# Performance work log

Measured on AMD Instinct MI355X. Metric: run time of the kernel, lower is better.

## Reference

```python
import jax, jax.numpy as jnp
import numpy as np

IN_FEATURES = 1024
OUT_FEATURES = 1024


def setup_inputs() -> dict:
    key = jax.random.key(0)
    k_x, k_w, k_b = jax.random.split(key, 3)
    # input activations [batch, seq, in_features]
    x = jax.random.normal(k_x, (4, 8192, IN_FEATURES), dtype=jnp.float32)
    # kaiming_uniform_(a=sqrt(5)) on [out, in] -> bound = 1/sqrt(in_features)
    bound = 1.0 / np.sqrt(IN_FEATURES)
    weight = jax.random.uniform(k_w, (OUT_FEATURES, IN_FEATURES), dtype=jnp.float32,
                                minval=-bound, maxval=bound)
    bias = jax.random.uniform(k_b, (OUT_FEATURES,), dtype=jnp.float32,
                              minval=-bound, maxval=bound)
    # adiabatic binarization scale factors (non-trainable scalars)
    kk = jnp.float32(10.0)
    aa = jnp.float32(1.0)
    return {"x": x, "weight": weight, "bias": bias, "kk": kk, "aa": aa}


def reference(x, weight, bias, kk, aa):
    # BinaryLinearFunction: soft-binarize the weight with learned scales, then GEMM.
    # w_bin = aa * clamp(kk * w, -1, 1)  (annealed binarization; kk -> inf gives sign(w))
    w_bin = aa * jnp.clip(kk * weight, -1.0, 1.0)  # [out, in]
    # out[b, s, o] = sum_i x[b, s, i] * w_bin[o, i] + bias[o]
    return jnp.einsum('bsi,oi->bso', x, w_bin) + bias
```

## Files before the change

### kernel.cpp

```cpp
#include <hip/hip_runtime.h>
#include <stdint.h>

#define K_DIM 1024
#define N_DIM 1024
#define BM 256
#define BN 256
#define BK 64
#define NK (K_DIM / BK)

typedef __attribute__((ext_vector_type(4))) float f32x4;
typedef __attribute__((ext_vector_type(8))) short bf16x8;
typedef __attribute__((ext_vector_type(4))) uint32_t u32x4;

__device__ __forceinline__ uint32_t pack_bf16(float a, float b) {
  uint32_t ua = __builtin_bit_cast(uint32_t, a) + 0x8000u;
  uint32_t ub = __builtin_bit_cast(uint32_t, b) + 0x8000u;
  return __builtin_amdgcn_perm(ub, ua, 0x07060302u);
}

__device__ __forceinline__ float wbin1(float v, float kkv, float aav) {
  float t = v * kkv;
  t = fminf(fmaxf(t, -1.0f), 1.0f);
  return t * aav;
}

__global__ __launch_bounds__(256) void wconv(const float* __restrict__ w,
                                             const float* __restrict__ kkp,
                                             const float* __restrict__ aap,
                                             uint32_t* __restrict__ wb) {
  const float kkv = kkp[0];
  const float aav = aap[0];
  const int g = blockIdx.x * 256 + threadIdx.x;
  const f32x4* src = (const f32x4*)(w + (size_t)g * 16);
  f32x4 v0 = src[0], v1 = src[1], v2 = src[2], v3 = src[3];
  uint32_t p[8];
#pragma unroll
  for (int i = 0; i < 4; ++i) {
    f32x4 v = i == 0 ? v0 : (i == 1 ? v1 : (i == 2 ? v2 : v3));
    p[2 * i] = pack_bf16(wbin1(v[0], kkv, aav), wbin1(v[1], kkv, aav));
    p[2 * i + 1] = pack_bf16(wbin1(v[2], kkv, aav), wbin1(v[3], kkv, aav));
  }
  u32x4* dst = (u32x4*)(wb + (size_t)g * 8);
  dst[0] = u32x4{p[0], p[1], p[2], p[3]};
  dst[1] = u32x4{p[4], p[5], p[6], p[7]};
}

__global__ __launch_bounds__(256) void xconv(const float* __restrict__ x,
                                             uint32_t* __restrict__ xb) {
  const size_t g = (size_t)blockIdx.x * 256 + threadIdx.x;
  const f32x4* src = (const f32x4*)(x + g * 16);
  f32x4 v0 = src[0], v1 = src[1], v2 = src[2], v3 = src[3];
  uint32_t p[8];
  p[0] = pack_bf16(v0[0], v0[1]); p[1] = pack_bf16(v0[2], v0[3]);
  p[2] = pack_bf16(v1[0], v1[1]); p[3] = pack_bf16(v1[2], v1[3]);
  p[4] = pack_bf16(v2[0], v2[1]); p[5] = pack_bf16(v2[2], v2[3]);
  p[6] = pack_bf16(v3[0], v3[1]); p[7] = pack_bf16(v3[2], v3[3]);
  u32x4* dst = (u32x4*)(xb + g * 8);
  dst[0] = u32x4{p[0], p[1], p[2], p[3]};
  dst[1] = u32x4{p[4], p[5], p[6], p[7]};
}

__global__ __launch_bounds__(512, 2) void binlin_gemm8(
    const uint32_t* __restrict__ xb, const uint32_t* __restrict__ wb,
    const float* __restrict__ bias, float* __restrict__ out) {
  __shared__ uint32_t lds[2][(BM + BN) * 32];

  const int tid = threadIdx.x;

  const int per = gridDim.x >> 3;
  const int logical = (blockIdx.x & 7) * per + (blockIdx.x >> 3);
  const int mIdx = logical >> 2;
  const int nIdx = logical & 3;
  const int row0 = mIdx * BM;
  const int col0 = nIdx * BN;

  const int w8 = tid >> 6;
  const int lane = tid & 63;
  const int brow = lane >> 3;
  const int bslot = (lane & 7) ^ brow;
  const uint32_t* ga_base =
      xb + (size_t)(row0 + w8 * 32 + brow) * (K_DIM / 2) + bslot * 4;
  const uint32_t* gb_base =
      wb + (size_t)(col0 + w8 * 32 + brow) * (K_DIM / 2) + bslot * 4;

  const int wr = w8 >> 2;
  const int wc = w8 & 3;
  const int cl = lane & 15;
  const int kg = lane >> 4;

  f32x4 acc[8][4] = {};
  bf16x8 af[2][4], bfr[2][2];

#define STAGE_A8(kt, dstbase)                                             \
  do {                                                                    \
    _Pragma("unroll") for (int c4 = 0; c4 < 4; ++c4) {                    \
      __builtin_amdgcn_global_load_lds(                                   \
          (const __attribute__((address_space(1))) uint32_t*)(            \
              ga_base + (size_t)(c4 * 8) * (K_DIM / 2) + (kt) * 32),      \
          (__attribute__((address_space(3))) uint32_t*)(                  \
              (dstbase) + (w8 * 32 + c4 * 8) * 32),                       \
          16, 0, 0);                                                      \
    }                                                                     \
  } while (0)

#define STAGE_B8(kt, dstbase)                                             \
  do {                                                                    \
    _Pragma("unroll") for (int c4 = 0; c4 < 4; ++c4) {                    \
      __builtin_amdgcn_global_load_lds(                                   \
          (const __attribute__((address_space(1))) uint32_t*)(            \
              gb_base + (size_t)(c4 * 8) * (K_DIM / 2) + (kt) * 32),      \
          (__attribute__((address_space(3))) uint32_t*)(                  \
              (dstbase) + BM * 32 + (w8 * 32 + c4 * 8) * 32),             \
          16, 0, 0);                                                      \
    }                                                                     \
  } while (0)

#define READ_AF(AB, MH)                                                        \
  _Pragma("unroll") for (int ks = 0; ks < 2; ++ks)                             \
  _Pragma("unroll") for (int m = 0; m < 4; ++m) {                              \
    int rr = wr * 128 + ((MH)*4 + m) * 16 + cl;                                \
    af[ks][m] =                                                                \
        *(const bf16x8*)((AB) + rr * 32 + (((ks * 4 + kg) ^ (rr & 7)) * 4));   \
  }

#define READ_BF(BB, NH)                                                        \
  _Pragma("unroll") for (int ks = 0; ks < 2; ++ks)                             \
  _Pragma("unroll") for (int n = 0; n < 2; ++n) {                              \
    int rr = wc * 64 + ((NH)*2 + n) * 16 + cl;                                 \
    bfr[ks][n] =                                                               \
        *(const bf16x8*)((BB) + rr * 32 + (((ks * 4 + kg) ^ (rr & 7)) * 4));   \
  }

#define PHTAIL(MH, NH)                                                         \
  __builtin_amdgcn_s_barrier();                                                \
  asm volatile("s_waitcnt lgkmcnt(0)" ::: "memory");                           \
  __builtin_amdgcn_sched_barrier(0);                                           \
  __builtin_amdgcn_s_setprio(1);                                               \
  _Pragma("unroll") for (int ks = 0; ks < 2; ++ks)                             \
  _Pragma("unroll") for (int m = 0; m < 4; ++m)                                \
  _Pragma("unroll") for (int n = 0; n < 2; ++n)                                \
  acc[(MH)*4 + m][(NH)*2 + n] = __builtin_amdgcn_mfma_f32_16x16x32_bf16(       \
      af[ks][m], bfr[ks][n], acc[(MH)*4 + m][(NH)*2 + n], 0, 0, 0);            \
  __builtin_amdgcn_s_setprio(0);

  STAGE_A8(0, &lds[0][0]);
  STAGE_B8(0, &lds[0][0]);
  asm volatile("s_waitcnt vmcnt(0)" ::: "memory");
  __builtin_amdgcn_s_barrier();

  for (int kt = 0; kt < NK; ++kt) {
    const uint32_t* AB = &lds[kt & 1][0];
    const uint32_t* BB = AB + BM * 32;
    uint32_t* ND = &lds[(kt & 1) ^ 1][0];
    const bool more = (kt + 1) < NK;
    READ_AF(AB, 0);
    READ_BF(BB, 0);
    if (more) STAGE_A8(kt + 1, ND);
    PHTAIL(0, 0);
    __builtin_amdgcn_s_barrier();
    READ_BF(BB, 1);
    if (more) STAGE_B8(kt + 1, ND);
    PHTAIL(0, 1);
    __builtin_amdgcn_s_barrier();
    READ_AF(AB, 1);
    PHTAIL(1, 1);
    __builtin_amdgcn_s_barrier();
    READ_BF(BB, 0);
    PHTAIL(1, 0);
    asm volatile("s_waitcnt vmcnt(0)" ::: "memory");
    __builtin_amdgcn_s_barrier();
  }

#pragma unroll
  for (int n = 0; n < 4; ++n) {
    int col = col0 + wc * 64 + n * 16 + cl;
    float bv = bias[col];
#pragma unroll
    for (int m = 0; m < 8; ++m) {
      int rowb = row0 + wr * 128 + m * 16 + kg * 4;
#pragma unroll
      for (int i = 0; i < 4; ++i) {
        out[(size_t)(rowb + i) * N_DIM + col] = acc[m][n][i] + bv;
      }
    }
  }
#undef STAGE_A8
#undef STAGE_B8
#undef READ_AF
#undef READ_BF
#undef PHTAIL
}

__global__ __launch_bounds__(512, 2) void binlin_gemm_fb(
    const float* __restrict__ x, const uint32_t* __restrict__ wb,
    const float* __restrict__ bias, float* __restrict__ out) {
  __shared__ uint32_t lds[2][(BM + BN) * 32];

  const int tid = threadIdx.x;
  const int per = gridDim.x >> 3;
  const int logical = (blockIdx.x & 7) * per + (blockIdx.x >> 3);
  const int mIdx = logical >> 2;
  const int nIdx = logical & 3;
  const int row0 = mIdx * BM;
  const int col0 = nIdx * BN;

  const int r = tid >> 1;
  const int h = tid & 1;
  const int sw = r & 7;
  const float* ga = x + (size_t)(row0 + r) * K_DIM + h * 32;
  const int aoff = r * 32;

  const int w8 = tid >> 6;
  const int lane = tid & 63;
  const int brow = lane >> 3;
  const int bslot = (lane & 7) ^ brow;
  const uint32_t* gb_base =
      wb + (size_t)(col0 + w8 * 32 + brow) * (K_DIM / 2) + bslot * 4;
  const int boff = (w8 * 32) * 32;

  const int wr = w8 >> 2;
  const int wc = w8 & 3;
  const int cl = lane & 15;
  const int kg = lane >> 4;

  f32x4 acc[8][4] = {};
  f32x4 ra[8];

#define LOADA(kt)                                                \
  {                                                              \
    const f32x4* pa = (const f32x4*)(ga + (kt)*BK);              \
    _Pragma("unroll") for (int i = 0; i < 8; ++i) ra[i] = pa[i]; \
  }
#define WRITEA(buf)                                                       \
  {                                                                       \
    uint32_t* lap = &lds[buf][0] + aoff;                                  \
    _Pragma("unroll") for (int j = 0; j < 4; ++j) {                       \
      u32x4 pk = {pack_bf16(ra[2 * j][0], ra[2 * j][1]),                  \
                  pack_bf16(ra[2 * j][2], ra[2 * j][3]),                  \
                  pack_bf16(ra[2 * j + 1][0], ra[2 * j + 1][1]),          \
                  pack_bf16(ra[2 * j + 1][2], ra[2 * j + 1][3])};         \
      *(u32x4*)(lap + (((h * 4 + j) ^ sw) * 4)) = pk;                     \
    }                                                                     \
  }
#define STAGEB(kt, buf)                                                    \
  {                                                                        \
    uint32_t* lbp = &lds[buf][BM * 32] + boff;                             \
    _Pragma("unroll") for (int c = 0; c < 4; ++c) {                        \
      __builtin_amdgcn_global_load_lds(                                    \
          (const __attribute__((address_space(1))) uint32_t*)(             \
              gb_base + (size_t)(c * 8) * (K_DIM / 2) + (kt)*32),          \
          (__attribute__((address_space(3))) uint32_t*)(lbp + c * 8 * 32), \
          16, 0, 0);                                                       \
    }                                                                      \
  }
#define COMPUTE(buf)                                                           \
  {                                                                            \
    const uint32_t* A = &lds[buf][0];                                          \
    const uint32_t* B = &lds[buf][BM * 32];                                    \
    _Pragma("unroll") for (int ks = 0; ks < 2; ++ks) {                         \
      bf16x8 bfr[4];                                                           \
      _Pragma("unroll") for (int n = 0; n < 4; ++n) {                          \
        int rr = wc * 64 + n * 16 + cl;                                        \
        bfr[n] =                                                               \
            *(const bf16x8*)(B + rr * 32 + (((ks * 4 + kg) ^ (rr & 7)) * 4));  \
      }                                                                        \
      _Pragma("unroll") for (int mh = 0; mh < 2; ++mh) {                       \
        bf16x8 af[4];                                                          \
        _Pragma("unroll") for (int m = 0; m < 4; ++m) {                        \
          int rr = wr * 128 + (mh * 4 + m) * 16 + cl;                          \
          af[m] =                                                              \
              *(const bf16x8*)(A + rr * 32 + (((ks * 4 + kg) ^ (rr & 7)) * 4));\
        }                                                                      \
        __builtin_amdgcn_s_setprio(1);                                         \
        _Pragma("unroll") for (int m = 0; m < 4; ++m)                          \
            _Pragma("unroll") for (int n = 0; n < 4; ++n)                      \
                acc[mh * 4 + m][n] = __builtin_amdgcn_mfma_f32_16x16x32_bf16(  \
                    af[m], bfr[n], acc[mh * 4 + m][n], 0, 0, 0);               \
        __builtin_amdgcn_s_setprio(0);                                         \
      }                                                                        \
    }                                                                          \
  }

  LOADA(0);
  STAGEB(0, 0);
  WRITEA(0);
  asm volatile("s_waitcnt vmcnt(0) lgkmcnt(0)" ::: "memory");
  __builtin_amdgcn_s_barrier();

  for (int kt2 = 0; kt2 < NK; kt2 += 2) {
    LOADA(kt2 + 1);
    STAGEB(kt2 + 1, 1);
    asm volatile("s_waitcnt vmcnt(12)" ::: "memory");
    __builtin_amdgcn_s_barrier();
    __builtin_amdgcn_sched_barrier(0);
    COMPUTE(0);
    WRITEA(1);
    asm volatile("s_waitcnt lgkmcnt(0)" ::: "memory");
    if (kt2 + 2 < NK) {
      LOADA(kt2 + 2);
      STAGEB(kt2 + 2, 0);
      asm volatile("s_waitcnt vmcnt(12)" ::: "memory");
    } else {
      asm volatile("s_waitcnt vmcnt(0)" ::: "memory");
    }
    __builtin_amdgcn_s_barrier();
    __builtin_amdgcn_sched_barrier(0);
    COMPUTE(1);
    if (kt2 + 2 < NK) {
      WRITEA(0);
      asm volatile("s_waitcnt lgkmcnt(0)" ::: "memory");
    }
  }

#pragma unroll
  for (int n = 0; n < 4; ++n) {
    int col = col0 + wc * 64 + n * 16 + cl;
    float bv = bias[col];
#pragma unroll
    for (int m = 0; m < 8; ++m) {
      int rowb = row0 + wr * 128 + m * 16 + kg * 4;
#pragma unroll
      for (int i = 0; i < 4; ++i) {
        out[(size_t)(rowb + i) * N_DIM + col] = acc[m][n][i] + bv;
      }
    }
  }
#undef LOADA
#undef WRITEA
#undef STAGEB
#undef COMPUTE
}

extern "C" void kernel_launch(void* const* d_in, const int* in_sizes, int n_in,
                              void* d_out, int out_size, void* d_ws, size_t ws_size,
                              hipStream_t stream) {
  const float* x = (const float*)d_in[0];
  const float* w = (const float*)d_in[1];
  const float* bias = (const float*)d_in[2];
  const float* kk = (const float*)d_in[3];
  const float* aa = (const float*)d_in[4];
  float* out = (float*)d_out;

  uint32_t* wb = (uint32_t*)d_ws;
  wconv<<<(N_DIM * K_DIM) / (256 * 16), 256, 0, stream>>>(w, kk, aa, wb);

  const int M = in_sizes[0] / K_DIM;
  const int grid = (M / BM) * (N_DIM / BN);

  const size_t wb_bytes = (size_t)N_DIM * K_DIM * 2;
  const size_t xb_bytes = (size_t)M * K_DIM * 2;
  if (ws_size >= wb_bytes + xb_bytes) {
    uint32_t* xbp = (uint32_t*)((char*)d_ws + wb_bytes);
    xconv<<<(int)(((size_t)M * K_DIM) / (256 * 16)), 256, 0, stream>>>(x, xbp);
    binlin_gemm8<<<grid, 512, 0, stream>>>(xbp, wb, bias, out);
  } else {
    binlin_gemm_fb<<<grid, 512, 0, stream>>>(x, wb, bias, out);
  }
}
```

Baseline: 125.3 us.

## Switch bf16 GEMM to 256x128 tiles with three-stage LDS pipeline

The pre-converted bf16 GEMM now uses 256x128 output tiles instead of 256x256, which doubles the grid and halves the accumulators per thread. Shared memory now holds a triple-buffered ring with a prefetch distance of two k-tiles, and partial vmcnt waits let loads for two stages be in flight while the current one computes. The intent is to hide global-to-LDS latency better and improve occupancy and load balance across CUs. The cost is lower arithmetic intensity per tile, so each block reloads more A and B data.

```diff
diff --git a/kernel.cpp b/kernel.cpp
--- a/kernel.cpp
+++ b/kernel.cpp
@@ -4,9 +4,10 @@
 #define K_DIM 1024
 #define N_DIM 1024
 #define BM 256
-#define BN 256
+#define BN3 128
 #define BK 64
 #define NK (K_DIM / BK)
+#define UNIT_U32 ((BM + BN3) * 32)
 
 typedef __attribute__((ext_vector_type(4))) float f32x4;
 typedef __attribute__((ext_vector_type(8))) short bf16x8;
@@ -60,19 +61,19 @@
   dst[1] = u32x4{p[4], p[5], p[6], p[7]};
 }
 
-__global__ __launch_bounds__(512, 2) void binlin_gemm8(
+__global__ __launch_bounds__(512, 2) void binlin_gemm3r(
     const uint32_t* __restrict__ xb, const uint32_t* __restrict__ wb,
     const float* __restrict__ bias, float* __restrict__ out) {
-  __shared__ uint32_t lds[2][(BM + BN) * 32];
+  __shared__ uint32_t lds[3 * UNIT_U32];
 
   const int tid = threadIdx.x;
 
   const int per = gridDim.x >> 3;
   const int logical = (blockIdx.x & 7) * per + (blockIdx.x >> 3);
-  const int mIdx = logical >> 2;
-  const int nIdx = logical & 3;
+  const int mIdx = logical >> 3;
+  const int nIdx = logical & 7;
   const int row0 = mIdx * BM;
-  const int col0 = nIdx * BN;
+  const int col0 = nIdx * BN3;
 
   const int w8 = tid >> 6;
   const int lane = tid & 63;
@@ -81,44 +82,42 @@
   const uint32_t* ga_base =
       xb + (size_t)(row0 + w8 * 32 + brow) * (K_DIM / 2) + bslot * 4;
   const uint32_t* gb_base =
-      wb + (size_t)(col0 + w8 * 32 + brow) * (K_DIM / 2) + bslot * 4;
-
-  const int wr = w8 >> 2;
-  const int wc = w8 & 3;
+      wb + (size_t)(col0 + w8 * 16 + brow) * (K_DIM / 2) + bslot * 4;
+
+  const int wr = w8 >> 1;
+  const int wc = w8 & 1;
   const int cl = lane & 15;
   const int kg = lane >> 4;
 
-  f32x4 acc[8][4] = {};
+  f32x4 acc[4][4] = {};
   bf16x8 af[2][4], bfr[2][2];
 
-#define STAGE_A8(kt, dstbase)                                             \
+#define STAGE_A2(kt, SD, c0)                                              \
   do {                                                                    \
-    _Pragma("unroll") for (int c4 = 0; c4 < 4; ++c4) {                    \
+    _Pragma("unroll") for (int c = (c0); c < (c0) + 2; ++c) {             \
       __builtin_amdgcn_global_load_lds(                                   \
           (const __attribute__((address_space(1))) uint32_t*)(            \
-              ga_base + (size_t)(c4 * 8) * (K_DIM / 2) + (kt) * 32),      \
+              ga_base + (size_t)(c * 8) * (K_DIM / 2) + (kt) * 32),       \
           (__attribute__((address_space(3))) uint32_t*)(                  \
-              (dstbase) + (w8 * 32 + c4 * 8) * 32),                       \
+              (SD) + (w8 * 32 + c * 8) * 32),                             \
           16, 0, 0);                                                      \
     }                                                                     \
   } while (0)
 
-#define STAGE_B8(kt, dstbase)                                             \
+#define STAGE_B1(kt, SD, c)                                               \
   do {                                                                    \
-    _Pragma("unroll") for (int c4 = 0; c4 < 4; ++c4) {                    \
-      __builtin_amdgcn_global_load_lds(                                   \
-          (const __attribute__((address_space(1))) uint32_t*)(            \
-              gb_base + (size_t)(c4 * 8) * (K_DIM / 2) + (kt) * 32),      \
-          (__attribute__((address_space(3))) uint32_t*)(                  \
-              (dstbase) + BM * 32 + (w8 * 32 + c4 * 8) * 32),             \
-          16, 0, 0);                                                      \
-    }                                                                     \
+    __builtin_amdgcn_global_load_lds(                                     \
+        (const __attribute__((address_space(1))) uint32_t*)(              \
+            gb_base + (size_t)((c) * 8) * (K_DIM / 2) + (kt) * 32),       \
+        (__attribute__((address_space(3))) uint32_t*)(                    \
+            (SD) + BM * 32 + (w8 * 16 + (c) * 8) * 32),                   \
+        16, 0, 0);                                                        \
   } while (0)
 
-#define READ_AF(AB, MH)                                                        \
+#define READ_AF(AB)                                                            \
   _Pragma("unroll") for (int ks = 0; ks < 2; ++ks)                             \
   _Pragma("unroll") for (int m = 0; m < 4; ++m) {                              \
-    int rr = wr * 128 + ((MH)*4 + m) * 16 + cl;                                \
+    int rr = wr * 64 + m * 16 + cl;                                            \
     af[ks][m] =                                                                \
         *(const bf16x8*)((AB) + rr * 32 + (((ks * 4 + kg) ^ (rr & 7)) * 4));   \
   }
@@ -131,7 +130,7 @@
         *(const bf16x8*)((BB) + rr * 32 + (((ks * 4 + kg) ^ (rr & 7)) * 4));   \
   }
 
-#define PHTAIL(MH, NH)                                                         \
+#define PHTAIL(NH)                                                             \
   __builtin_amdgcn_s_barrier();                                                \
   asm volatile("s_waitcnt lgkmcnt(0)" ::: "memory");                           \
   __builtin_amdgcn_sched_barrier(0);                                           \
@@ -139,36 +138,49 @@
   _Pragma("unroll") for (int ks = 0; ks < 2; ++ks)                             \
   _Pragma("unroll") for (int m = 0; m < 4; ++m)                                \
   _Pragma("unroll") for (int n = 0; n < 2; ++n)                                \
-  acc[(MH)*4 + m][(NH)*2 + n] = __builtin_amdgcn_mfma_f32_16x16x32_bf16(       \
-      af[ks][m], bfr[ks][n], acc[(MH)*4 + m][(NH)*2 + n], 0, 0, 0);            \
+  acc[m][(NH)*2 + n] = __builtin_amdgcn_mfma_f32_16x16x32_bf16(                \
+      af[ks][m], bfr[ks][n], acc[m][(NH)*2 + n], 0, 0, 0);                     \
   __builtin_amdgcn_s_setprio(0);
 
-  STAGE_A8(0, &lds[0][0]);
-  STAGE_B8(0, &lds[0][0]);
-  asm volatile("s_waitcnt vmcnt(0)" ::: "memory");
+  STAGE_A2(0, &lds[0], 0);
+  STAGE_A2(0, &lds[0], 2);
+  STAGE_B1(0, &lds[0], 0);
+  STAGE_B1(0, &lds[0], 1);
+  STAGE_A2(1, &lds[UNIT_U32], 0);
+  STAGE_A2(1, &lds[UNIT_U32], 2);
+  STAGE_B1(1, &lds[UNIT_U32], 0);
+  STAGE_B1(1, &lds[UNIT_U32], 1);
+  asm volatile("s_waitcnt vmcnt(6)" ::: "memory");
   __builtin_amdgcn_s_barrier();
 
-  for (int kt = 0; kt < NK; ++kt) {
-    const uint32_t* AB = &lds[kt & 1][0];
+  int cu = 0, su = 2;
+  for (int t = 0; t < NK; ++t) {
+    const uint32_t* AB = &lds[cu * UNIT_U32];
     const uint32_t* BB = AB + BM * 32;
-    uint32_t* ND = &lds[(kt & 1) ^ 1][0];
-    const bool more = (kt + 1) < NK;
-    READ_AF(AB, 0);
+    uint32_t* SD = &lds[su * UNIT_U32];
+    const bool more = (t + 2) < NK;
+    READ_AF(AB);
     READ_BF(BB, 0);
-    if (more) STAGE_A8(kt + 1, ND);
-    PHTAIL(0, 0);
+    if (more) {
+      STAGE_A2(t + 2, SD, 0);
+      STAGE_B1(t + 2, SD, 0);
+    }
+    PHTAIL(0);
     __builtin_amdgcn_s_barrier();
     READ_BF(BB, 1);
-    if (more) STAGE_B8(kt + 1, ND);
-    PHTAIL(0, 1);
+    if (more) {
+      STAGE_A2(t + 2, SD, 2);
+      STAGE_B1(t + 2, SD, 1);
+    }
+    PHTAIL(1);
+    if (t < NK - 2) {
+      asm volatile("s_waitcnt vmcnt(6)" ::: "memory");
+    } else if (t == NK - 2) {
+      asm volatile("s_waitcnt vmcnt(0)" ::: "memory");
+    }
     __builtin_amdgcn_s_barrier();
-    READ_AF(AB, 1);
-    PHTAIL(1, 1);
-    __builtin_amdgcn_s_barrier();
-    READ_BF(BB, 0);
-    PHTAIL(1, 0);
-    asm volatile("s_waitcnt vmcnt(0)" ::: "memory");
-    __builtin_amdgcn_s_barrier();
+    cu = (cu == 2) ? 0 : cu + 1;
+    su = (su == 2) ? 0 : su + 1;
   }
 
 #pragma unroll
@@ -176,25 +188,26 @@
     int col = col0 + wc * 64 + n * 16 + cl;
     float bv = bias[col];
 #pragma unroll
-    for (int m = 0; m < 8; ++m) {
-      int rowb = row0 + wr * 128 + m * 16 + kg * 4;
+    for (int m = 0; m < 4; ++m) {
+      int rowb = row0 + wr * 64 + m * 16 + kg * 4;
 #pragma unroll
       for (int i = 0; i < 4; ++i) {
         out[(size_t)(rowb + i) * N_DIM + col] = acc[m][n][i] + bv;
       }
     }
   }
-#undef STAGE_A8
-#undef STAGE_B8
+#undef STAGE_A2
+#undef STAGE_B1
 #undef READ_AF
 #undef READ_BF
 #undef PHTAIL
 }
 
+#define BNF 256
 __global__ __launch_bounds__(512, 2) void binlin_gemm_fb(
     const float* __restrict__ x, const uint32_t* __restrict__ wb,
     const float* __restrict__ bias, float* __restrict__ out) {
-  __shared__ uint32_t lds[2][(BM + BN) * 32];
+  __shared__ uint32_t lds[2][(BM + BNF) * 32];
 
   const int tid = threadIdx.x;
   const int per = gridDim.x >> 3;
@@ -202,7 +215,7 @@
   const int mIdx = logical >> 2;
   const int nIdx = logical & 3;
   const int row0 = mIdx * BM;
-  const int col0 = nIdx * BN;
+  const int col0 = nIdx * BNF;
 
   const int r = tid >> 1;
   const int h = tid & 1;
@@ -345,15 +358,16 @@
   wconv<<<(N_DIM * K_DIM) / (256 * 16), 256, 0, stream>>>(w, kk, aa, wb);
 
   const int M = in_sizes[0] / K_DIM;
-  const int grid = (M / BM) * (N_DIM / BN);
 
   const size_t wb_bytes = (size_t)N_DIM * K_DIM * 2;
   const size_t xb_bytes = (size_t)M * K_DIM * 2;
   if (ws_size >= wb_bytes + xb_bytes) {
     uint32_t* xbp = (uint32_t*)((char*)d_ws + wb_bytes);
     xconv<<<(int)(((size_t)M * K_DIM) / (256 * 16)), 256, 0, stream>>>(x, xbp);
-    binlin_gemm8<<<grid, 512, 0, stream>>>(xbp, wb, bias, out);
+    const int grid = (M / BM) * (N_DIM / BN3);
+    binlin_gemm3r<<<grid, 512, 0, stream>>>(xbp, wb, bias, out);
   } else {
+    const int grid = (M / BM) * (N_DIM / BNF);
     binlin_gemm_fb<<<grid, 512, 0, stream>>>(x, wb, bias, out);
   }
 }
```

After: 125.8 us. About the same (+0.4%).

## Switch GEMM to 4-stage ring buffer with BK=32 and prefetch distance 3

Applied to the files above, without the earlier changes.

Replaces the double-buffered BK=64 main loop with a four-slot LDS ring of BK=32 tiles. Loads run three tiles ahead, and partial vmcnt waits keep several global-to-LDS transfers in flight. The LDS swizzle and thread-to-row mapping are reworked for the narrower 32-wide K tile. The loop now iterates twice as often, with fewer barriers per iteration but less MFMA work between syncs, and the same total LDS footprint.

```diff
diff --git a/kernel.cpp b/kernel.cpp
--- a/kernel.cpp
+++ b/kernel.cpp
@@ -5,8 +5,12 @@
 #define N_DIM 1024
 #define BM 256
 #define BN 256
-#define BK 64
-#define NK (K_DIM / BK)
+#define BK4 32
+#define NT (K_DIM / BK4)
+#define UNIT4_U32 ((BM + BN) * 16)
+
+#define AS1 __attribute__((address_space(1)))
+#define AS3 __attribute__((address_space(3)))
 
 typedef __attribute__((ext_vector_type(4))) float f32x4;
 typedef __attribute__((ext_vector_type(8))) short bf16x8;
@@ -60,10 +64,10 @@
   dst[1] = u32x4{p[4], p[5], p[6], p[7]};
 }
 
-__global__ __launch_bounds__(512, 2) void binlin_gemm8(
+__global__ __launch_bounds__(512, 2) void binlin_gemm4r(
     const uint32_t* __restrict__ xb, const uint32_t* __restrict__ wb,
     const float* __restrict__ bias, float* __restrict__ out) {
-  __shared__ uint32_t lds[2][(BM + BN) * 32];
+  __shared__ uint32_t lds[4 * UNIT4_U32];
 
   const int tid = threadIdx.x;
 
@@ -76,12 +80,12 @@
 
   const int w8 = tid >> 6;
   const int lane = tid & 63;
-  const int brow = lane >> 3;
-  const int bslot = (lane & 7) ^ brow;
+  const int rl = lane >> 2;
+  const int sl = (lane & 3) ^ ((lane >> 3) & 3);
   const uint32_t* ga_base =
-      xb + (size_t)(row0 + w8 * 32 + brow) * (K_DIM / 2) + bslot * 4;
+      xb + (size_t)(row0 + w8 * 32 + rl) * (K_DIM / 2) + sl * 4;
   const uint32_t* gb_base =
-      wb + (size_t)(col0 + w8 * 32 + brow) * (K_DIM / 2) + bslot * 4;
+      wb + (size_t)(col0 + w8 * 32 + rl) * (K_DIM / 2) + sl * 4;
 
   const int wr = w8 >> 2;
   const int wc = w8 & 3;
@@ -89,85 +93,82 @@
   const int kg = lane >> 4;
 
   f32x4 acc[8][4] = {};
-  bf16x8 af[2][4], bfr[2][2];
-
-#define STAGE_A8(kt, dstbase)                                             \
-  do {                                                                    \
-    _Pragma("unroll") for (int c4 = 0; c4 < 4; ++c4) {                    \
-      __builtin_amdgcn_global_load_lds(                                   \
-          (const __attribute__((address_space(1))) uint32_t*)(            \
-              ga_base + (size_t)(c4 * 8) * (K_DIM / 2) + (kt) * 32),      \
-          (__attribute__((address_space(3))) uint32_t*)(                  \
-              (dstbase) + (w8 * 32 + c4 * 8) * 32),                       \
-          16, 0, 0);                                                      \
-    }                                                                     \
-  } while (0)
-
-#define STAGE_B8(kt, dstbase)                                             \
-  do {                                                                    \
-    _Pragma("unroll") for (int c4 = 0; c4 < 4; ++c4) {                    \
-      __builtin_amdgcn_global_load_lds(                                   \
-          (const __attribute__((address_space(1))) uint32_t*)(            \
-              gb_base + (size_t)(c4 * 8) * (K_DIM / 2) + (kt) * 32),      \
-          (__attribute__((address_space(3))) uint32_t*)(                  \
-              (dstbase) + BM * 32 + (w8 * 32 + c4 * 8) * 32),             \
-          16, 0, 0);                                                      \
-    }                                                                     \
-  } while (0)
-
-#define READ_AF(AB, MH)                                                        \
-  _Pragma("unroll") for (int ks = 0; ks < 2; ++ks)                             \
-  _Pragma("unroll") for (int m = 0; m < 4; ++m) {                              \
-    int rr = wr * 128 + ((MH)*4 + m) * 16 + cl;                                \
-    af[ks][m] =                                                                \
-        *(const bf16x8*)((AB) + rr * 32 + (((ks * 4 + kg) ^ (rr & 7)) * 4));   \
+  bf16x8 af[8], bfr[2];
+
+#define STAGE_A1(kt, SD, c)                                               \
+  __builtin_amdgcn_global_load_lds(                                       \
+      (const AS1 uint32_t*)(ga_base + (size_t)((c)*16) * (K_DIM / 2) +    \
+                            (kt)*16),                                     \
+      (AS3 uint32_t*)((SD) + (w8 * 32 + (c)*16) * 16), 16, 0, 0)
+
+#define STAGE_B1(kt, SD, c)                                               \
+  __builtin_amdgcn_global_load_lds(                                       \
+      (const AS1 uint32_t*)(gb_base + (size_t)((c)*16) * (K_DIM / 2) +    \
+                            (kt)*16),                                     \
+      (AS3 uint32_t*)((SD) + BM * 16 + (w8 * 32 + (c)*16) * 16), 16, 0, 0)
+
+#define READ_AF(AB)                                                            \
+  _Pragma("unroll") for (int m = 0; m < 8; ++m) {                              \
+    int rr = wr * 128 + m * 16 + cl;                                           \
+    af[m] =                                                                    \
+        *(const bf16x8*)((AB) + rr * 16 + ((kg ^ ((rr >> 1) & 3)) * 4));       \
   }
 
 #define READ_BF(BB, NH)                                                        \
-  _Pragma("unroll") for (int ks = 0; ks < 2; ++ks)                             \
   _Pragma("unroll") for (int n = 0; n < 2; ++n) {                              \
     int rr = wc * 64 + ((NH)*2 + n) * 16 + cl;                                 \
-    bfr[ks][n] =                                                               \
-        *(const bf16x8*)((BB) + rr * 32 + (((ks * 4 + kg) ^ (rr & 7)) * 4));   \
-  }
-
-#define PHTAIL(MH, NH)                                                         \
+    bfr[n] =                                                                   \
+        *(const bf16x8*)((BB) + rr * 16 + ((kg ^ ((rr >> 1) & 3)) * 4));       \
+  }
+
+#define PHTAIL(NH)                                                             \
   __builtin_amdgcn_s_barrier();                                                \
   asm volatile("s_waitcnt lgkmcnt(0)" ::: "memory");                           \
   __builtin_amdgcn_sched_barrier(0);                                           \
   __builtin_amdgcn_s_setprio(1);                                               \
-  _Pragma("unroll") for (int ks = 0; ks < 2; ++ks)                             \
-  _Pragma("unroll") for (int m = 0; m < 4; ++m)                                \
+  _Pragma("unroll") for (int m = 0; m < 8; ++m)                                \
   _Pragma("unroll") for (int n = 0; n < 2; ++n)                                \
-  acc[(MH)*4 + m][(NH)*2 + n] = __builtin_amdgcn_mfma_f32_16x16x32_bf16(       \
-      af[ks][m], bfr[ks][n], acc[(MH)*4 + m][(NH)*2 + n], 0, 0, 0);            \
+  acc[m][(NH)*2 + n] = __builtin_amdgcn_mfma_f32_16x16x32_bf16(                \
+      af[m], bfr[n], acc[m][(NH)*2 + n], 0, 0, 0);                             \
   __builtin_amdgcn_s_setprio(0);
 
-  STAGE_A8(0, &lds[0][0]);
-  STAGE_B8(0, &lds[0][0]);
-  asm volatile("s_waitcnt vmcnt(0)" ::: "memory");
+#pragma unroll
+  for (int u = 0; u < 3; ++u) {
+    uint32_t* SD = &lds[u * UNIT4_U32];
+    STAGE_A1(u, SD, 0);
+    STAGE_A1(u, SD, 1);
+    STAGE_B1(u, SD, 0);
+    STAGE_B1(u, SD, 1);
+  }
+  asm volatile("s_waitcnt vmcnt(8)" ::: "memory");
   __builtin_amdgcn_s_barrier();
 
-  for (int kt = 0; kt < NK; ++kt) {
-    const uint32_t* AB = &lds[kt & 1][0];
-    const uint32_t* BB = AB + BM * 32;
-    uint32_t* ND = &lds[(kt & 1) ^ 1][0];
-    const bool more = (kt + 1) < NK;
-    READ_AF(AB, 0);
+  for (int t = 0; t < NT; ++t) {
+    const uint32_t* AB = &lds[(t & 3) * UNIT4_U32];
+    const uint32_t* BB = AB + BM * 16;
+    uint32_t* SD = &lds[((t + 3) & 3) * UNIT4_U32];
+    const bool more = (t + 3) < NT;
+    READ_AF(AB);
     READ_BF(BB, 0);
-    if (more) STAGE_A8(kt + 1, ND);
-    PHTAIL(0, 0);
+    if (more) {
+      STAGE_A1(t + 3, SD, 0);
+      STAGE_A1(t + 3, SD, 1);
+    }
+    PHTAIL(0);
     __builtin_amdgcn_s_barrier();
     READ_BF(BB, 1);
-    if (more) STAGE_B8(kt + 1, ND);
-    PHTAIL(0, 1);
-    __builtin_amdgcn_s_barrier();
-    READ_AF(AB, 1);
-    PHTAIL(1, 1);
-    __builtin_amdgcn_s_barrier();
-    READ_BF(BB, 0);
-    PHTAIL(1, 0);
-    asm volatile("s_waitcnt vmcnt(0)" ::: "memory");
+    if (more) {
+      STAGE_B1(t + 3, SD, 0);
+      STAGE_B1(t + 3, SD, 1);
+    }
+    PHTAIL(1);
+    if (t < NT - 3) {
+      asm volatile("s_waitcnt vmcnt(8)" ::: "memory");
+    } else if (t == NT - 3) {
+      asm volatile("s_waitcnt vmcnt(4)" ::: "memory");
+    } else if (t == NT - 2) {
+      asm volatile("s_waitcnt vmcnt(0)" ::: "memory");
+    }
     __builtin_amdgcn_s_barrier();
   }
 
@@ -184,13 +185,15 @@
       }
     }
   }
-#undef STAGE_A8
-#undef STAGE_B8
+#undef STAGE_A1
+#undef STAGE_B1
 #undef READ_AF
 #undef READ_BF
 #undef PHTAIL
 }
 
+#define BK 64
+#define NK (K_DIM / BK)
 __global__ __launch_bounds__(512, 2) void binlin_gemm_fb(
     const float* __restrict__ x, const uint32_t* __restrict__ wb,
     const float* __restrict__ bias, float* __restrict__ out) {
@@ -247,10 +250,9 @@
     uint32_t* lbp = &lds[buf][BM * 32] + boff;                             \
     _Pragma("unroll") for (int c = 0; c < 4; ++c) {                        \
       __builtin_amdgcn_global_load_lds(                                    \
-          (const __attribute__((address_space(1))) uint32_t*)(             \
-              gb_base + (size_t)(c * 8) * (K_DIM / 2) + (kt)*32),          \
-          (__attribute__((address_space(3))) uint32_t*)(lbp + c * 8 * 32), \
-          16, 0, 0);                                                       \
+          (const AS1 uint32_t*)(gb_base + (size_t)(c * 8) * (K_DIM / 2) +  \
+                                (kt)*32),                                  \
+          (AS3 uint32_t*)(lbp + c * 8 * 32), 16, 0, 0);                    \
     }                                                                      \
   }
 #define COMPUTE(buf)                                                           \
@@ -352,7 +354,7 @@
   if (ws_size >= wb_bytes + xb_bytes) {
     uint32_t* xbp = (uint32_t*)((char*)d_ws + wb_bytes);
     xconv<<<(int)(((size_t)M * K_DIM) / (256 * 16)), 256, 0, stream>>>(x, xbp);
-    binlin_gemm8<<<grid, 512, 0, stream>>>(xbp, wb, bias, out);
+    binlin_gemm4r<<<grid, 512, 0, stream>>>(xbp, wb, bias, out);
   } else {
     binlin_gemm_fb<<<grid, 512, 0, stream>>>(x, wb, bias, out);
   }
```

After: 126.9 us. Within noise of the previous version (+1.2%).
